# Kernel tuning notes

Hardware: AMD Instinct MI355X
Metric: run time of the kernel (lower is better)

The kernel has to match this reference:

```python
import jax, jax.numpy as jnp
import numpy as np

EPS = 1e-12


def setup_inputs() -> dict:
    key = jax.random.key(0)
    k1, k2, k3 = jax.random.split(key, 3)
    N, H, W, D, K = 32, 64, 64, 512, 116
    x = jax.random.normal(k1, (N, H, W, D), dtype=jnp.float32)
    conv_w = jax.random.normal(k2, (D, K), dtype=jnp.float32) * 0.05
    C = jax.random.normal(k3, (D, K), dtype=jnp.float32) * 0.05
    return {"x": x, "conv_w": conv_w, "C": C}


def reference(x, conv_w, C):
    # x: (N,H,W,D); conv_w: (D,K) 1x1-conv kernel; C: (D,K) cluster centers.
    # Assignment logits via 1x1 conv == matmul over channels.
    s = jnp.einsum('nhwd,dk->nhwk', x, conv_w)          # (N,H,W,K)
    a = jax.nn.softmax(s, axis=-1)                      # softmax over clusters
    # Algebraic decomposition of sum_{h,w} a[...,k] * (x[...,d] + C[d,k]):
    ax = jnp.einsum('nhwk,nhwd->ndk', a, x)             # (N,D,K)
    asum = jnp.sum(a, axis=(1, 2))                      # (N,K)
    v = ax + C[None, :, :] * asum[:, None, :]           # (N,D,K)
    # Intra-normalization: after transpose to (N,K,D) the norm is over D.
    v = v / jnp.sqrt(jnp.sum(v * v, axis=1, keepdims=True) + EPS)
    # Flatten in (N, D, K) row-major order (matches tf transpose-back + Flatten).
    v = v.reshape(v.shape[0], -1)                       # (N, D*K)
    v = v / jnp.sqrt(jnp.sum(v * v, axis=-1, keepdims=True) + EPS)
    return v
```

## Files before the change

### kernel.cpp

```cpp
#include <hip/hip_runtime.h>
#include <hip/hip_bf16.h>

#define EPS_F 1e-12f

typedef __attribute__((ext_vector_type(8))) short bf16x8;
typedef __attribute__((ext_vector_type(4))) float f32x4;

__device__ __forceinline__ unsigned short f2bf(float f) {
    __hip_bfloat16 h = __float2bfloat16(f);
    unsigned short u; __builtin_memcpy(&u, &h, 2); return u;
}


__global__ void wt_prep(const float* __restrict__ w,
                        unsigned short* __restrict__ WT) {
    int id = blockIdx.x * 256 + threadIdx.x;
    int k = id >> 9, d = id & 511;
    WT[k * 512 + d] = (k < 116) ? f2bf(w[d * 116 + k]) : (unsigned short)0;
}

__global__ __launch_bounds__(256, 2)
void assign_k(const float* __restrict__ x,
              const unsigned short* __restrict__ WT,
              unsigned short* __restrict__ At,
              float* __restrict__ asum) {
    __shared__ unsigned short sm[27648];
    unsigned short* Xs = sm;
    unsigned short* Ws = sm + 18432;
    const int tid = threadIdx.x;
    const int wave = tid >> 6, lane = tid & 63;
    const int quad = lane >> 4, l15 = lane & 15;
    const int pxbase = blockIdx.x * 256;
    const int n = pxbase >> 12;

    f32x4 acc[4][8];
#pragma unroll
    for (int s = 0; s < 4; ++s)
#pragma unroll
        for (int c = 0; c < 8; ++c) acc[s][c] = (f32x4){0.f, 0.f, 0.f, 0.f};

    for (int dch = 0; dch < 8; ++dch) {
        const int dof = dch * 64;
#pragma unroll
        for (int it = 0; it < 16; ++it) {
            int cid = it * 256 + tid;
            int r = cid >> 4, co = (cid & 15) * 4;
            float4 v = *(const float4*)(x + (size_t)(pxbase + r) * 512 + dof + co);
            ushort4 u;
            u.x = f2bf(v.x); u.y = f2bf(v.y); u.z = f2bf(v.z); u.w = f2bf(v.w);
            *(ushort4*)(Xs + r * 72 + co) = u;
        }
#pragma unroll
        for (int i = 0; i < 4; ++i) {
            int cid = i * 256 + tid;
            int r = cid >> 3, co = (cid & 7) * 8;
            uint4 v = *(const uint4*)(WT + r * 512 + dof + co);
            *(uint4*)(Ws + r * 72 + co) = v;
        }
        __syncthreads();
#pragma unroll
        for (int ks = 0; ks < 2; ++ks) {
            const int ko = ks * 32 + quad * 8;
            bf16x8 af[4], bfr[8];
#pragma unroll
            for (int s = 0; s < 4; ++s)
                af[s] = *(const bf16x8*)(Xs + (wave * 64 + s * 16 + l15) * 72 + ko);
#pragma unroll
            for (int c = 0; c < 8; ++c)
                bfr[c] = *(const bf16x8*)(Ws + (c * 16 + l15) * 72 + ko);
#pragma unroll
            for (int s = 0; s < 4; ++s)
#pragma unroll
                for (int c = 0; c < 8; ++c)
                    acc[s][c] = __builtin_amdgcn_mfma_f32_16x16x32_bf16(
                        af[s], bfr[c], acc[s][c], 0, 0, 0);
        }
        __syncthreads();
    }

    const bool v7 = (l15 < 4);
#pragma unroll
    for (int s = 0; s < 4; ++s) {
#pragma unroll
        for (int r = 0; r < 4; ++r) {
            float mx = acc[s][0][r];
#pragma unroll
            for (int c = 1; c < 7; ++c) mx = fmaxf(mx, acc[s][c][r]);
            if (v7) mx = fmaxf(mx, acc[s][7][r]);
#pragma unroll
            for (int off = 1; off < 16; off <<= 1) mx = fmaxf(mx, __shfl_xor(mx, off));
            float sum = 0.f;
#pragma unroll
            for (int c = 0; c < 8; ++c) {
                float e = (c < 7 || v7) ? __expf(acc[s][c][r] - mx) : 0.f;
                acc[s][c][r] = e; sum += e;
            }
#pragma unroll
            for (int off = 1; off < 16; off <<= 1) sum += __shfl_xor(sum, off);
            float inv = 1.0f / sum;
#pragma unroll
            for (int c = 0; c < 8; ++c) acc[s][c][r] *= inv;
        }
    }

#pragma unroll
    for (int c = 0; c < 8; ++c) {
        float cs = 0.f;
#pragma unroll
        for (int s = 0; s < 4; ++s)
#pragma unroll
            for (int r = 0; r < 4; ++r) cs += acc[s][c][r];
        cs += __shfl_xor(cs, 16);
        cs += __shfl_xor(cs, 32);
        int k = c * 16 + l15;
        if (lane < 16 && k < 116) atomicAdd(asum + n * 128 + k, cs);
    }

    __syncthreads();
    unsigned short* tb = sm + wave * 4608;
    const int pw = (pxbase & 4095) + wave * 64;
#pragma unroll
    for (int ch = 0; ch < 2; ++ch) {
#pragma unroll
        for (int c4 = 0; c4 < 4; ++c4) {
            int c = ch * 4 + c4;
            int kk = c4 * 16 + l15;
#pragma unroll
            for (int s = 0; s < 4; ++s) {
                ushort4 u;
                u.x = f2bf(acc[s][c][0]); u.y = f2bf(acc[s][c][1]);
                u.z = f2bf(acc[s][c][2]); u.w = f2bf(acc[s][c][3]);
                *(ushort4*)(tb + kk * 72 + s * 16 + quad * 4) = u;
            }
        }
#pragma unroll
        for (int it = 0; it < 8; ++it) {
            int id = it * 64 + lane;
            int row = id >> 3, chk = id & 7;
            uint4 v = *(const uint4*)(tb + row * 72 + chk * 8);
            *(uint4*)(At + (size_t)(n * 128 + ch * 64 + row) * 4096 + pw + chk * 8) = v;
        }
    }
}

__global__ __launch_bounds__(256, 2)
void ax_k(const float* __restrict__ x,
          const unsigned short* __restrict__ At,
          float* __restrict__ ax0, float* __restrict__ ax1) {
    __shared__ unsigned short sm[13824];
    unsigned short* Ats = sm;
    unsigned short* Xts = sm + 9216;
    const int tid = threadIdx.x;
    const int wave = tid >> 6, lane = tid & 63;
    const int quad = lane >> 4, l15 = lane & 15;
    const int bid = blockIdx.x;
    const int xcd = bid & 7, slot = bid >> 3;
    const int dblk = slot & 7, ghi = slot >> 3;
    const int g = ghi * 8 + xcd;
    const int n = g >> 1, ps = g & 1;
    const int dbase = dblk * 64;
    const int p0 = ps * 2048;

    f32x4 acc[2][4];
#pragma unroll
    for (int s = 0; s < 2; ++s)
#pragma unroll
        for (int c = 0; c < 4; ++c) acc[s][c] = (f32x4){0.f, 0.f, 0.f, 0.f};

    for (int pc = 0; pc < 32; ++pc) {
        const int pb = p0 + pc * 64;
#pragma unroll
        for (int i = 0; i < 4; ++i) {
            int cid = i * 256 + tid;
            int r = cid >> 3, co = (cid & 7) * 8;
            uint4 v = *(const uint4*)(At + (size_t)(n * 128 + r) * 4096 + pb + co);
            *(uint4*)(Ats + r * 72 + co) = v;
        }
        {
            const float* xrow = x + (size_t)(n * 4096 + pb + lane) * 512 + dbase + wave * 16;
#pragma unroll
            for (int f = 0; f < 4; ++f) {
                float4 v = *(const float4*)(xrow + f * 4);
                int dl = wave * 16 + f * 4;
                Xts[(dl + 0) * 72 + lane] = f2bf(v.x);
                Xts[(dl + 1) * 72 + lane] = f2bf(v.y);
                Xts[(dl + 2) * 72 + lane] = f2bf(v.z);
                Xts[(dl + 3) * 72 + lane] = f2bf(v.w);
            }
        }
        __syncthreads();
#pragma unroll
        for (int ks = 0; ks < 2; ++ks) {
            const int ko = ks * 32 + quad * 8;
            bf16x8 af[2], bfr[4];
            af[0] = *(const bf16x8*)(Ats + (wave * 32 + l15) * 72 + ko);
            af[1] = *(const bf16x8*)(Ats + (wave * 32 + 16 + l15) * 72 + ko);
#pragma unroll
            for (int c = 0; c < 4; ++c)
                bfr[c] = *(const bf16x8*)(Xts + (c * 16 + l15) * 72 + ko);
#pragma unroll
            for (int s = 0; s < 2; ++s)
#pragma unroll
                for (int c = 0; c < 4; ++c)
                    acc[s][c] = __builtin_amdgcn_mfma_f32_16x16x32_bf16(
                        af[s], bfr[c], acc[s][c], 0, 0, 0);
        }
        __syncthreads();
    }

    float* axp = ps ? ax1 : ax0;
#pragma unroll
    for (int s = 0; s < 2; ++s)
#pragma unroll
        for (int c = 0; c < 4; ++c) {
            int d = dbase + c * 16 + l15;
            int k = wave * 32 + s * 16 + quad * 4;
            *(f32x4*)(axp + (size_t)(n * 512 + d) * 128 + k) = acc[s][c];
        }
}

__global__ void ss_k(const float* __restrict__ ax0, const float* __restrict__ ax1,
                     const float* __restrict__ C,
                     const float* __restrict__ asum, float* __restrict__ ssb) {
    __shared__ float red[256];
    const int tid = threadIdx.x;
    const int n = blockIdx.x >> 3, dgrp = blockIdx.x & 7;
    const int k = tid & 127, dh = tid >> 7;
    const float as = asum[n * 128 + k];
    float ssq = 0.f;
    for (int i = 0; i < 32; ++i) {
        int d = dgrp * 64 + i * 2 + dh;
        size_t ix = (size_t)(n * 512 + d) * 128 + k;
        float cc = (k < 116) ? C[d * 116 + k] : 0.f;
        float v = ax0[ix] + ax1[ix] + cc * as;
        ssq += v * v;
    }
    red[tid] = ssq;
    __syncthreads();
    if (dh == 0) atomicAdd(ssb + n * 128 + k, red[tid] + red[tid + 128]);
}

__global__ void scale_k(const float* __restrict__ ssb, float* __restrict__ scl) {
    __shared__ float red[128];
    const int n = blockIdx.x, k = threadIdx.x;
    const float s = ssb[n * 128 + k];
    red[k] = (k < 116) ? (s / (s + EPS_F)) : 0.f;
    __syncthreads();
    for (int off = 64; off > 0; off >>= 1) {
        if (k < off) red[k] += red[k + off];
        __syncthreads();
    }
    float rowinv = rsqrtf(red[0] + EPS_F);
    scl[n * 128 + k] = rsqrtf(s + EPS_F) * rowinv;
}

__global__ void emit_k(const float* __restrict__ ax0, const float* __restrict__ ax1,
                       const float* __restrict__ C,
                       const float* __restrict__ asum, const float* __restrict__ scl,
                       float* __restrict__ out) {
    const int n = blockIdx.x >> 3, dgrp = blockIdx.x & 7;
    const int tid = threadIdx.x;
    for (int i = 0; i < 29; ++i) {
        int idx = i * 256 + tid;
        int dl = idx / 116;
        int k = idx - dl * 116;
        int d = dgrp * 64 + dl;
        size_t ix = (size_t)(n * 512 + d) * 128 + k;
        float v = ax0[ix] + ax1[ix] + C[d * 116 + k] * asum[n * 128 + k];
        out[(size_t)n * 59392 + dgrp * 7424 + idx] = v * scl[n * 128 + k];
    }
}

extern "C" void kernel_launch(void* const* d_in, const int* in_sizes, int n_in,
                              void* d_out, int out_size, void* d_ws, size_t ws_size,
                              hipStream_t stream) {
    const float* x = (const float*)d_in[0];
    const float* w = (const float*)d_in[1];
    const float* C = (const float*)d_in[2];
    float* out = (float*)d_out;

    char* ws = (char*)d_ws;
    unsigned short* At  = (unsigned short*)ws;
    float* ax0  = (float*)(ws + 33554432);
    float* ax1  = (float*)(ws + 41943040);
    float* asum = (float*)(ws + 50331648);
    float* ssb  = (float*)(ws + 50348032);
    float* scl  = (float*)(ws + 50364416);
    unsigned short* WT = (unsigned short*)(ws + 50380800);

    hipMemsetAsync(ws + 50331648, 0, 32768, stream);

    wt_prep <<<256, 256, 0, stream>>>(w, WT);
    assign_k<<<512, 256, 0, stream>>>(x, WT, At, asum);
    ax_k    <<<512, 256, 0, stream>>>(x, At, ax0, ax1);
    ss_k    <<<256, 256, 0, stream>>>(ax0, ax1, C, asum, ssb);
    scale_k <<<32, 128, 0, stream>>>(ssb, scl);
    emit_k  <<<256, 256, 0, stream>>>(ax0, ax1, C, asum, scl, out);
}
```

Baseline: 513.5 us.

## Fuse assignment softmax and aggregation GEMMs into one kernel reading x once

Merges the assignment GEMM plus softmax kernel and the aggregation GEMM kernel into one fused kernel. It converts a 64-pixel tile of x to bf16 in shared memory once and reuses it for both the logits and the a^T·x product, and keeps the softmax weights in LDS. This drops the bf16 assignment matrix round trip through global memory and the second full read of x. Each block covers 512 pixels, so partial sums go to the single ax buffer through float atomics. That adds atomic traffic and a larger memset, and the grid shrinks to 256 blocks of 512 threads, which may cut parallelism.

```diff
diff --git a/kernel.cpp b/kernel.cpp
--- a/kernel.cpp
+++ b/kernel.cpp
@@ -19,208 +19,189 @@
     WT[k * 512 + d] = (k < 116) ? f2bf(w[d * 116 + k]) : (unsigned short)0;
 }
 
-__global__ __launch_bounds__(256, 2)
-void assign_k(const float* __restrict__ x,
-              const unsigned short* __restrict__ WT,
-              unsigned short* __restrict__ At,
-              float* __restrict__ asum) {
-    __shared__ unsigned short sm[27648];
-    unsigned short* Xs = sm;
-    unsigned short* Ws = sm + 18432;
+__global__ __launch_bounds__(512, 2)
+void fused_k(const float* __restrict__ x, const unsigned short* __restrict__ WT,
+             float* __restrict__ ax, float* __restrict__ asum) {
+    __shared__ __align__(16) unsigned short xs[32768];
+    __shared__ __align__(16) unsigned short aTs[128 * 72];
+    __shared__ __align__(16) float smax[64 * 12];
+    __shared__ __align__(16) float ssum[64 * 12];
+
     const int tid = threadIdx.x;
     const int wave = tid >> 6, lane = tid & 63;
-    const int quad = lane >> 4, l15 = lane & 15;
-    const int pxbase = blockIdx.x * 256;
-    const int n = pxbase >> 12;
-
-    f32x4 acc[4][8];
-#pragma unroll
-    for (int s = 0; s < 4; ++s)
-#pragma unroll
-        for (int c = 0; c < 8; ++c) acc[s][c] = (f32x4){0.f, 0.f, 0.f, 0.f};
-
-    for (int dch = 0; dch < 8; ++dch) {
-        const int dof = dch * 64;
-#pragma unroll
-        for (int it = 0; it < 16; ++it) {
-            int cid = it * 256 + tid;
-            int r = cid >> 4, co = (cid & 15) * 4;
-            float4 v = *(const float4*)(x + (size_t)(pxbase + r) * 512 + dof + co);
+    const int q = lane >> 4, l15 = lane & 15;
+    const int n = blockIdx.x >> 3;
+    const int pb = (blockIdx.x & 7) << 9;
+    const int kk = wave * 16 + l15;
+    const bool kvalid = kk < 116;
+
+    bf16x8 wt[16];
+    {
+        const unsigned short* wp = WT + (size_t)kk * 512 + q * 8;
+#pragma unroll
+        for (int kc = 0; kc < 16; ++kc) wt[kc] = *(const bf16x8*)(wp + kc * 32);
+    }
+
+    f32x4 acc2[8][4];
+#pragma unroll
+    for (int a = 0; a < 8; ++a)
+#pragma unroll
+        for (int b = 0; b < 4; ++b) acc2[a][b] = (f32x4){0.f, 0.f, 0.f, 0.f};
+    float asr = 0.f;
+
+    const int sd = wave * 64 + (lane >> 2) * 4;
+    const float* xbase = x + (size_t)(n * 4096 + pb) * 512 + sd;
+    const int wbase = (sd >> 4) * 128 + (lane & 3) * 32 + (sd & 15) * 2;
+
+    for (int t = 0; t < 8; ++t) {
+        {
+            const float* xt = xbase + (size_t)(t * 64 + (lane & 3)) * 512;
+            float4 vb[8];
+#pragma unroll
+            for (int half = 0; half < 2; ++half) {
+#pragma unroll
+                for (int i = 0; i < 8; ++i)
+                    vb[i] = *(const float4*)(xt + (size_t)(half * 8 + i) * 2048);
+#pragma unroll
+                for (int i = 0; i < 8; ++i) {
+                    ushort4 u;
+                    u.x = f2bf(vb[i].x); u.y = f2bf(vb[i].y);
+                    u.z = f2bf(vb[i].z); u.w = f2bf(vb[i].w);
+                    *(ushort4*)((char*)xs + wbase + (half * 8 + i) * 4096) = u;
+                }
+            }
+        }
+        __syncthreads();
+
+        f32x4 s1[4];
+#pragma unroll
+        for (int pt = 0; pt < 4; ++pt) s1[pt] = (f32x4){0.f, 0.f, 0.f, 0.f};
+        {
+            const int abase = (l15 >> 2) * 4096 + (l15 & 3) * 32 +
+                              (q >> 1) * 128 + (q & 1) * 16;
+#pragma unroll
+            for (int kc = 0; kc < 16; ++kc)
+#pragma unroll
+                for (int pt = 0; pt < 4; ++pt) {
+                    bf16x8 af = *(const bf16x8*)((char*)xs + abase +
+                                                 pt * 16384 + kc * 256);
+                    s1[pt] = __builtin_amdgcn_mfma_f32_16x16x32_bf16(
+                        af, wt[kc], s1[pt], 0, 0, 0);
+                }
+        }
+
+        float mx[4][4];
+#pragma unroll
+        for (int pt = 0; pt < 4; ++pt)
+#pragma unroll
+            for (int r = 0; r < 4; ++r)
+                mx[pt][r] = kvalid ? s1[pt][r] : -3.0e38f;
+#pragma unroll
+        for (int off = 1; off < 16; off <<= 1)
+#pragma unroll
+            for (int pt = 0; pt < 4; ++pt)
+#pragma unroll
+                for (int r = 0; r < 4; ++r)
+                    mx[pt][r] = fmaxf(mx[pt][r], __shfl_xor(mx[pt][r], off));
+        if (l15 == 0) {
+#pragma unroll
+            for (int pt = 0; pt < 4; ++pt)
+#pragma unroll
+                for (int r = 0; r < 4; ++r)
+                    smax[(pt * 16 + q * 4 + r) * 12 + wave] = mx[pt][r];
+        }
+        __syncthreads();
+
+        float sm[4][4];
+#pragma unroll
+        for (int pt = 0; pt < 4; ++pt)
+#pragma unroll
+            for (int r = 0; r < 4; ++r) {
+                const float* mp = smax + (pt * 16 + q * 4 + r) * 12;
+                f32x4 a0 = *(const f32x4*)mp;
+                f32x4 b0 = *(const f32x4*)(mp + 4);
+                float M = fmaxf(fmaxf(fmaxf(a0[0], a0[1]), fmaxf(a0[2], a0[3])),
+                                fmaxf(fmaxf(b0[0], b0[1]), fmaxf(b0[2], b0[3])));
+                float e0 = kvalid ? __expf(s1[pt][r] - M) : 0.f;
+                s1[pt][r] = e0;
+                sm[pt][r] = e0;
+            }
+#pragma unroll
+        for (int off = 1; off < 16; off <<= 1)
+#pragma unroll
+            for (int pt = 0; pt < 4; ++pt)
+#pragma unroll
+                for (int r = 0; r < 4; ++r)
+                    sm[pt][r] += __shfl_xor(sm[pt][r], off);
+        if (l15 == 0) {
+#pragma unroll
+            for (int pt = 0; pt < 4; ++pt)
+#pragma unroll
+                for (int r = 0; r < 4; ++r)
+                    ssum[(pt * 16 + q * 4 + r) * 12 + wave] = sm[pt][r];
+        }
+        __syncthreads();
+
+#pragma unroll
+        for (int pt = 0; pt < 4; ++pt) {
+            float av[4];
+#pragma unroll
+            for (int r = 0; r < 4; ++r) {
+                const float* sp = ssum + (pt * 16 + q * 4 + r) * 12;
+                f32x4 a0 = *(const f32x4*)sp;
+                f32x4 b0 = *(const f32x4*)(sp + 4);
+                float S = (a0[0] + a0[1] + a0[2] + a0[3]) +
+                          (b0[0] + b0[1] + b0[2] + b0[3]);
+                av[r] = s1[pt][r] * (1.0f / S);
+                asr += av[r];
+            }
             ushort4 u;
-            u.x = f2bf(v.x); u.y = f2bf(v.y); u.z = f2bf(v.z); u.w = f2bf(v.w);
-            *(ushort4*)(Xs + r * 72 + co) = u;
-        }
-#pragma unroll
-        for (int i = 0; i < 4; ++i) {
-            int cid = i * 256 + tid;
-            int r = cid >> 3, co = (cid & 7) * 8;
-            uint4 v = *(const uint4*)(WT + r * 512 + dof + co);
-            *(uint4*)(Ws + r * 72 + co) = v;
-        }
-        __syncthreads();
-#pragma unroll
-        for (int ks = 0; ks < 2; ++ks) {
-            const int ko = ks * 32 + quad * 8;
-            bf16x8 af[4], bfr[8];
-#pragma unroll
-            for (int s = 0; s < 4; ++s)
-                af[s] = *(const bf16x8*)(Xs + (wave * 64 + s * 16 + l15) * 72 + ko);
-#pragma unroll
-            for (int c = 0; c < 8; ++c)
-                bfr[c] = *(const bf16x8*)(Ws + (c * 16 + l15) * 72 + ko);
-#pragma unroll
-            for (int s = 0; s < 4; ++s)
-#pragma unroll
-                for (int c = 0; c < 8; ++c)
-                    acc[s][c] = __builtin_amdgcn_mfma_f32_16x16x32_bf16(
-                        af[s], bfr[c], acc[s][c], 0, 0, 0);
-        }
-        __syncthreads();
-    }
-
-    const bool v7 = (l15 < 4);
-#pragma unroll
-    for (int s = 0; s < 4; ++s) {
-#pragma unroll
-        for (int r = 0; r < 4; ++r) {
-            float mx = acc[s][0][r];
-#pragma unroll
-            for (int c = 1; c < 7; ++c) mx = fmaxf(mx, acc[s][c][r]);
-            if (v7) mx = fmaxf(mx, acc[s][7][r]);
-#pragma unroll
-            for (int off = 1; off < 16; off <<= 1) mx = fmaxf(mx, __shfl_xor(mx, off));
-            float sum = 0.f;
-#pragma unroll
-            for (int c = 0; c < 8; ++c) {
-                float e = (c < 7 || v7) ? __expf(acc[s][c][r] - mx) : 0.f;
-                acc[s][c][r] = e; sum += e;
-            }
-#pragma unroll
-            for (int off = 1; off < 16; off <<= 1) sum += __shfl_xor(sum, off);
-            float inv = 1.0f / sum;
-#pragma unroll
-            for (int c = 0; c < 8; ++c) acc[s][c][r] *= inv;
-        }
-    }
-
-#pragma unroll
-    for (int c = 0; c < 8; ++c) {
-        float cs = 0.f;
-#pragma unroll
-        for (int s = 0; s < 4; ++s)
-#pragma unroll
-            for (int r = 0; r < 4; ++r) cs += acc[s][c][r];
-        cs += __shfl_xor(cs, 16);
-        cs += __shfl_xor(cs, 32);
-        int k = c * 16 + l15;
-        if (lane < 16 && k < 116) atomicAdd(asum + n * 128 + k, cs);
-    }
-
-    __syncthreads();
-    unsigned short* tb = sm + wave * 4608;
-    const int pw = (pxbase & 4095) + wave * 64;
-#pragma unroll
-    for (int ch = 0; ch < 2; ++ch) {
-#pragma unroll
-        for (int c4 = 0; c4 < 4; ++c4) {
-            int c = ch * 4 + c4;
-            int kk = c4 * 16 + l15;
-#pragma unroll
-            for (int s = 0; s < 4; ++s) {
-                ushort4 u;
-                u.x = f2bf(acc[s][c][0]); u.y = f2bf(acc[s][c][1]);
-                u.z = f2bf(acc[s][c][2]); u.w = f2bf(acc[s][c][3]);
-                *(ushort4*)(tb + kk * 72 + s * 16 + quad * 4) = u;
-            }
-        }
-#pragma unroll
-        for (int it = 0; it < 8; ++it) {
-            int id = it * 64 + lane;
-            int row = id >> 3, chk = id & 7;
-            uint4 v = *(const uint4*)(tb + row * 72 + chk * 8);
-            *(uint4*)(At + (size_t)(n * 128 + ch * 64 + row) * 4096 + pw + chk * 8) = v;
-        }
-    }
-}
-
-__global__ __launch_bounds__(256, 2)
-void ax_k(const float* __restrict__ x,
-          const unsigned short* __restrict__ At,
-          float* __restrict__ ax0, float* __restrict__ ax1) {
-    __shared__ unsigned short sm[13824];
-    unsigned short* Ats = sm;
-    unsigned short* Xts = sm + 9216;
-    const int tid = threadIdx.x;
-    const int wave = tid >> 6, lane = tid & 63;
-    const int quad = lane >> 4, l15 = lane & 15;
-    const int bid = blockIdx.x;
-    const int xcd = bid & 7, slot = bid >> 3;
-    const int dblk = slot & 7, ghi = slot >> 3;
-    const int g = ghi * 8 + xcd;
-    const int n = g >> 1, ps = g & 1;
-    const int dbase = dblk * 64;
-    const int p0 = ps * 2048;
-
-    f32x4 acc[2][4];
-#pragma unroll
-    for (int s = 0; s < 2; ++s)
-#pragma unroll
-        for (int c = 0; c < 4; ++c) acc[s][c] = (f32x4){0.f, 0.f, 0.f, 0.f};
-
-    for (int pc = 0; pc < 32; ++pc) {
-        const int pb = p0 + pc * 64;
-#pragma unroll
-        for (int i = 0; i < 4; ++i) {
-            int cid = i * 256 + tid;
-            int r = cid >> 3, co = (cid & 7) * 8;
-            uint4 v = *(const uint4*)(At + (size_t)(n * 128 + r) * 4096 + pb + co);
-            *(uint4*)(Ats + r * 72 + co) = v;
-        }
-        {
-            const float* xrow = x + (size_t)(n * 4096 + pb + lane) * 512 + dbase + wave * 16;
-#pragma unroll
-            for (int f = 0; f < 4; ++f) {
-                float4 v = *(const float4*)(xrow + f * 4);
-                int dl = wave * 16 + f * 4;
-                Xts[(dl + 0) * 72 + lane] = f2bf(v.x);
-                Xts[(dl + 1) * 72 + lane] = f2bf(v.y);
-                Xts[(dl + 2) * 72 + lane] = f2bf(v.z);
-                Xts[(dl + 3) * 72 + lane] = f2bf(v.w);
-            }
-        }
-        __syncthreads();
-#pragma unroll
-        for (int ks = 0; ks < 2; ++ks) {
-            const int ko = ks * 32 + quad * 8;
-            bf16x8 af[2], bfr[4];
-            af[0] = *(const bf16x8*)(Ats + (wave * 32 + l15) * 72 + ko);
-            af[1] = *(const bf16x8*)(Ats + (wave * 32 + 16 + l15) * 72 + ko);
-#pragma unroll
-            for (int c = 0; c < 4; ++c)
-                bfr[c] = *(const bf16x8*)(Xts + (c * 16 + l15) * 72 + ko);
-#pragma unroll
-            for (int s = 0; s < 2; ++s)
-#pragma unroll
-                for (int c = 0; c < 4; ++c)
-                    acc[s][c] = __builtin_amdgcn_mfma_f32_16x16x32_bf16(
-                        af[s], bfr[c], acc[s][c], 0, 0, 0);
-        }
-        __syncthreads();
-    }
-
-    float* axp = ps ? ax1 : ax0;
-#pragma unroll
-    for (int s = 0; s < 2; ++s)
-#pragma unroll
-        for (int c = 0; c < 4; ++c) {
-            int d = dbase + c * 16 + l15;
-            int k = wave * 32 + s * 16 + quad * 4;
-            *(f32x4*)(axp + (size_t)(n * 512 + d) * 128 + k) = acc[s][c];
-        }
-}
-
-__global__ void ss_k(const float* __restrict__ ax0, const float* __restrict__ ax1,
-                     const float* __restrict__ C,
+            u.x = f2bf(av[0]); u.y = f2bf(av[1]);
+            u.z = f2bf(av[2]); u.w = f2bf(av[3]);
+            *(ushort4*)(aTs + kk * 72 + pt * 16 + q * 4) = u;
+        }
+        __syncthreads();
+
+#pragma unroll
+        for (int pc = 0; pc < 2; ++pc) {
+            bf16x8 Bv[4];
+#pragma unroll
+            for (int dt = 0; dt < 4; ++dt) {
+                const int eb = (pc * 8 + q * 2) * 2048 + (wave * 4 + dt) * 64 + l15;
+#pragma unroll
+                for (int j = 0; j < 8; ++j)
+                    Bv[dt][j] = (short)xs[eb + (j >> 2) * 2048 + (j & 3) * 16];
+            }
+#pragma unroll
+            for (int kt = 0; kt < 8; ++kt) {
+                bf16x8 A = *(const bf16x8*)(aTs + (kt * 16 + l15) * 72 +
+                                            pc * 32 + q * 8);
+#pragma unroll
+                for (int dt = 0; dt < 4; ++dt)
+                    acc2[kt][dt] = __builtin_amdgcn_mfma_f32_16x16x32_bf16(
+                        A, Bv[dt], acc2[kt][dt], 0, 0, 0);
+            }
+        }
+        __syncthreads();
+    }
+
+#pragma unroll
+    for (int kt = 0; kt < 8; ++kt)
+#pragma unroll
+        for (int dt = 0; dt < 4; ++dt) {
+            const int d = wave * 64 + dt * 16 + l15;
+            float* pp = ax + ((size_t)(n * 512 + d) << 7) + kt * 16 + q * 4;
+            atomicAdd(pp + 0, acc2[kt][dt][0]);
+            atomicAdd(pp + 1, acc2[kt][dt][1]);
+            atomicAdd(pp + 2, acc2[kt][dt][2]);
+            atomicAdd(pp + 3, acc2[kt][dt][3]);
+        }
+    asr += __shfl_xor(asr, 16);
+    asr += __shfl_xor(asr, 32);
+    if (lane < 16 && kvalid) atomicAdd(asum + n * 128 + kk, asr);
+}
+
+__global__ void ss_k(const float* __restrict__ ax, const float* __restrict__ C,
                      const float* __restrict__ asum, float* __restrict__ ssb) {
     __shared__ float red[256];
     const int tid = threadIdx.x;
@@ -232,7 +213,7 @@
         int d = dgrp * 64 + i * 2 + dh;
         size_t ix = (size_t)(n * 512 + d) * 128 + k;
         float cc = (k < 116) ? C[d * 116 + k] : 0.f;
-        float v = ax0[ix] + ax1[ix] + cc * as;
+        float v = ax[ix] + cc * as;
         ssq += v * v;
     }
     red[tid] = ssq;
@@ -254,8 +235,7 @@
     scl[n * 128 + k] = rsqrtf(s + EPS_F) * rowinv;
 }
 
-__global__ void emit_k(const float* __restrict__ ax0, const float* __restrict__ ax1,
-                       const float* __restrict__ C,
+__global__ void emit_k(const float* __restrict__ ax, const float* __restrict__ C,
                        const float* __restrict__ asum, const float* __restrict__ scl,
                        float* __restrict__ out) {
     const int n = blockIdx.x >> 3, dgrp = blockIdx.x & 7;
@@ -266,7 +246,7 @@
         int k = idx - dl * 116;
         int d = dgrp * 64 + dl;
         size_t ix = (size_t)(n * 512 + d) * 128 + k;
-        float v = ax0[ix] + ax1[ix] + C[d * 116 + k] * asum[n * 128 + k];
+        float v = ax[ix] + C[d * 116 + k] * asum[n * 128 + k];
         out[(size_t)n * 59392 + dgrp * 7424 + idx] = v * scl[n * 128 + k];
     }
 }
@@ -280,20 +260,17 @@
     float* out = (float*)d_out;
 
     char* ws = (char*)d_ws;
-    unsigned short* At  = (unsigned short*)ws;
-    float* ax0  = (float*)(ws + 33554432);
-    float* ax1  = (float*)(ws + 41943040);
-    float* asum = (float*)(ws + 50331648);
-    float* ssb  = (float*)(ws + 50348032);
-    float* scl  = (float*)(ws + 50364416);
-    unsigned short* WT = (unsigned short*)(ws + 50380800);
-
-    hipMemsetAsync(ws + 50331648, 0, 32768, stream);
-
-    wt_prep <<<256, 256, 0, stream>>>(w, WT);
-    assign_k<<<512, 256, 0, stream>>>(x, WT, At, asum);
-    ax_k    <<<512, 256, 0, stream>>>(x, At, ax0, ax1);
-    ss_k    <<<256, 256, 0, stream>>>(ax0, ax1, C, asum, ssb);
-    scale_k <<<32, 128, 0, stream>>>(ssb, scl);
-    emit_k  <<<256, 256, 0, stream>>>(ax0, ax1, C, asum, scl, out);
-}
+    float* ax   = (float*)ws;
+    float* asum = (float*)(ws + 8388608);
+    float* ssb  = (float*)(ws + 8404992);
+    float* scl  = (float*)(ws + 8421376);
+    unsigned short* WT = (unsigned short*)(ws + 8437760);
+
+    hipMemsetAsync(ws, 0, 8421376, stream);
+
+    wt_prep<<<256, 256, 0, stream>>>(w, WT);
+    fused_k<<<256, 512, 0, stream>>>(x, WT, ax, asum);
+    ss_k   <<<256, 256, 0, stream>>>(ax, C, asum, ssb);
+    scale_k<<<32, 128, 0, stream>>>(ssb, scl);
+    emit_k <<<256, 256, 0, stream>>>(ax, C, asum, scl, out);
+}
```

Measured after the change: 646.1 us. 25.8% more time.
